# Optimization experiments

Measured on AMD Instinct MI355X. Metric: run time of the kernel, lower is better.

## Reference

```python
import jax, jax.numpy as jnp
import numpy as np
from jax import lax

EPS = 1e-3  # Keras BatchNormalization default epsilon
DN = ('NHWC', 'HWIO', 'NHWC')


def _bn(x, gamma, beta, mean, var):
    inv = gamma * lax.rsqrt(var + EPS)
    return x * inv + (beta - mean * inv)


def setup_inputs() -> dict:
    key = jax.random.key(0)
    ks = jax.random.split(key, 5)
    B, H, W, C = 32, 56, 56, 256
    G, CG = 32, 4  # cardinality, channels per group
    CM = G * CG    # 128 mid channels
    x = jax.random.normal(ks[0], (B, H, W, C), jnp.float32)
    # 32 branch 1x1 convs (256->4 each) stacked -> one 256->128 conv
    w1 = jax.random.normal(ks[1], (1, 1, C, CM), jnp.float32) * 0.05
    b1 = jnp.zeros((CM,), jnp.float32)
    g1 = jnp.ones((CM,), jnp.float32)
    be1 = jnp.zeros((CM,), jnp.float32)
    m1 = jnp.zeros((CM,), jnp.float32)
    v1 = jnp.ones((CM,), jnp.float32)
    # 32 branch 3x3 convs (4->4 each) stacked -> grouped conv kernel [3,3,4,128]
    w2 = jax.random.normal(ks[2], (3, 3, CG, CM), jnp.float32) * 0.1
    b2 = jnp.zeros((CM,), jnp.float32)
    g2 = jnp.ones((CM,), jnp.float32)
    be2 = jnp.zeros((CM,), jnp.float32)
    m2 = jnp.zeros((CM,), jnp.float32)
    v2 = jnp.ones((CM,), jnp.float32)
    # final 1x1 conv 128 -> 256
    w3 = jax.random.normal(ks[3], (1, 1, CM, C), jnp.float32) * 0.05
    b3 = jnp.zeros((C,), jnp.float32)
    return dict(x=x, w1=w1, b1=b1, g1=g1, be1=be1, m1=m1, v1=v1,
                w2=w2, b2=b2, g2=g2, be2=be2, m2=m2, v2=v2,
                w3=w3, b3=b3)


def reference(x, w1, b1, g1, be1, m1, v1, w2, b2, g2, be2, m2, v2, w3, b3):
    # branch 1x1 convs fused: conv 256 -> 128
    h = lax.conv_general_dilated(x, w1, (1, 1), 'SAME', dimension_numbers=DN) + b1
    h = jax.nn.relu(_bn(h, g1, be1, m1, v1))
    # branch 3x3 convs fused: grouped conv, 32 groups of 4 channels
    h = lax.conv_general_dilated(h, w2, (1, 1), 'SAME', dimension_numbers=DN,
                                 feature_group_count=32) + b2
    h = jax.nn.relu(_bn(h, g2, be2, m2, v2))
    # Dropout(0.2) is identity at inference
    # final 1x1 conv 128 -> 256, residual add, relu
    out = lax.conv_general_dilated(h, w3, (1, 1), 'SAME', dimension_numbers=DN) + b3
    return jax.nn.relu(out + x)
```

## Files before the change

### kernel.cpp

```cpp
#include <hip/hip_runtime.h>
#include <stdint.h>

typedef unsigned short u16;
typedef unsigned int   u32;
typedef __attribute__((ext_vector_type(8))) short bf16x8;
typedef __attribute__((ext_vector_type(4))) float f32x4;

#define EPS 1e-3f
#define NB 32
#define HW 56
#define CI 256
#define CM 128
#define PIX (NB*HW*HW)

__device__ __forceinline__ float asf(u32 i){ union{u32 u; float f;} t; t.u=i; return t.f; }
__device__ __forceinline__ u16 f2bf(float f){
  union{float f; u32 u;} t; t.f = f;
  u32 x = t.u;
  return (u16)((x + 0x7fffu + ((x>>16)&1u)) >> 16);
}

__global__ __launch_bounds__(256) void kprep(
    const float* __restrict__ w1, const float* __restrict__ b1, const float* __restrict__ g1,
    const float* __restrict__ be1, const float* __restrict__ m1, const float* __restrict__ v1,
    const float* __restrict__ b2, const float* __restrict__ g2,
    const float* __restrict__ be2, const float* __restrict__ m2, const float* __restrict__ v2,
    const float* __restrict__ w3,
    u16* __restrict__ w1t, u16* __restrict__ w3t,
    float* __restrict__ A1, float* __restrict__ B1,
    float* __restrict__ A2, float* __restrict__ B2){
  int i = blockIdx.x*256 + threadIdx.x;
  if (i < 32768){
    { int n = i >> 8, k = i & 255; w1t[i] = f2bf(w1[k*CM + n]); }
    { int n = i >> 7, k = i & 127; w3t[i] = f2bf(w3[k*CI + n]); }
  }
  if (i < 128){
    float s1 = g1[i] * rsqrtf(v1[i] + EPS);
    A1[i] = s1;
    B1[i] = b1[i]*s1 + be1[i] - m1[i]*s1;
    float s2 = g2[i] * rsqrtf(v2[i] + EPS);
    A2[i] = s2;
    B2[i] = b2[i]*s2 + be2[i] - m2[i]*s2;
  }
}

#define K1_LS 72
__global__ __launch_bounds__(256) void k1(const float* __restrict__ x,
    const u16* __restrict__ w1t, const float* __restrict__ A1v,
    const float* __restrict__ B1v, u16* __restrict__ h1){
  __shared__ __align__(16) char smem[64*K1_LS*2 + 128*K1_LS*2];
  u16* As = (u16*)smem;
  u16* Bs = (u16*)(smem + 64*K1_LS*2);
  const int tid  = threadIdx.x;
  const int lane = tid & 63, wv = tid >> 6;
  const int col  = lane & 15, quad = lane >> 4;
  const long p0 = (long)blockIdx.x * 64;
  f32x4 acc[4][2];
  #pragma unroll
  for (int a = 0; a < 4; a++){
    #pragma unroll
    for (int b = 0; b < 2; b++){ acc[a][b][0]=0.f; acc[a][b][1]=0.f; acc[a][b][2]=0.f; acc[a][b][3]=0.f; }
  }
  for (int kc = 0; kc < 4; kc++){
    #pragma unroll
    for (int r = 0; r < 4; r++){
      int idx = r*256 + tid;
      int m = idx >> 4, f4 = idx & 15;
      float4 v = *(const float4*)(x + (p0+m)*CI + kc*64 + f4*4);
      u32 lo = (u32)f2bf(v.x) | ((u32)f2bf(v.y) << 16);
      u32 hi = (u32)f2bf(v.z) | ((u32)f2bf(v.w) << 16);
      *(uint2*)(As + m*K1_LS + f4*4) = make_uint2(lo, hi);
    }
    #pragma unroll
    for (int r = 0; r < 4; r++){
      int idx = r*256 + tid;
      int n = idx >> 3, u4 = idx & 7;
      uint4 v = *(const uint4*)(w1t + n*CI + kc*64 + u4*8);
      *(uint4*)(Bs + n*K1_LS + u4*8) = v;
    }
    __syncthreads();
    #pragma unroll
    for (int ks = 0; ks < 2; ks++){
      bf16x8 af[4], bfr[2];
      #pragma unroll
      for (int mt = 0; mt < 4; mt++)
        af[mt] = *(const bf16x8*)(As + (mt*16 + col)*K1_LS + ks*32 + quad*8);
      #pragma unroll
      for (int nt = 0; nt < 2; nt++)
        bfr[nt] = *(const bf16x8*)(Bs + (wv*32 + nt*16 + col)*K1_LS + ks*32 + quad*8);
      #pragma unroll
      for (int mt = 0; mt < 4; mt++){
        #pragma unroll
        for (int nt = 0; nt < 2; nt++)
          acc[mt][nt] = __builtin_amdgcn_mfma_f32_16x16x32_bf16(af[mt], bfr[nt], acc[mt][nt], 0, 0, 0);
      }
    }
    __syncthreads();
  }
  u16* outw = (u16*)smem;
  #pragma unroll
  for (int nt = 0; nt < 2; nt++){
    int n = wv*32 + nt*16 + col;
    float a1 = A1v[n], b1v = B1v[n];
    #pragma unroll
    for (int mt = 0; mt < 4; mt++){
      #pragma unroll
      for (int reg = 0; reg < 4; reg++){
        int m = mt*16 + quad*4 + reg;
        outw[m*136 + n] = f2bf(fmaxf(acc[mt][nt][reg]*a1 + b1v, 0.f));
      }
    }
  }
  __syncthreads();
  #pragma unroll
  for (int r = 0; r < 4; r++){
    int idx = r*256 + tid;
    int m = idx >> 4, u4 = idx & 15;
    uint4 v = *(const uint4*)(outw + m*136 + u4*8);
    *(uint4*)(h1 + (p0+m)*CM + u4*8) = v;
  }
}

#define TW 58
#define CPAD 132
__global__ __launch_bounds__(256) void k2(const u16* __restrict__ h1,
    const float* __restrict__ wf2, const float* __restrict__ A2v,
    const float* __restrict__ B2v, u16* __restrict__ h2){
  __shared__ u16 tile[3][TW][CPAD];
  __shared__ float wsh[9*4*CM];
  const int tid = threadIdx.x;
  const int img = blockIdx.x / HW, y = blockIdx.x % HW;
  for (int i = tid; i < 4608; i += 256) wsh[i] = wf2[i];
  #pragma unroll
  for (int r = 0; r < 3; r++){
    const int yy = y + r - 1;
    if (yy < 0 || yy >= HW){
      u32* t = (u32*)&tile[r][0][0];
      for (int i = tid; i < TW*CPAD/2; i += 256) t[i] = 0u;
    } else {
      if (tid < CPAD){ tile[r][0][tid] = 0; tile[r][TW-1][tid] = 0; }
      const uint4* src = (const uint4*)(h1 + (size_t)(img*HW + yy)*HW*CM);
      for (int i = tid; i < 896; i += 256){
        uint4 v = src[i];
        int px = i >> 4, ch = (i & 15)*8;
        u16* d = &tile[r][px+1][ch];
        *(uint2*)d     = make_uint2(v.x, v.y);
        *(uint2*)(d+4) = make_uint2(v.z, v.w);
      }
    }
  }
  __syncthreads();
  const int lane = tid & 63, wv = tid >> 6;
  if (lane >= HW) return;
  const int px = lane;
  float acc[8][4];
  u16 ov[32];
  for (int gi = 0; gi < 8; gi++){
    const int cb = (wv*8 + gi)*4;
    float a0=0.f, a1=0.f, a2=0.f, a3=0.f;
    #pragma unroll
    for (int ky = 0; ky < 3; ky++){
      #pragma unroll
      for (int kx = 0; kx < 3; kx++){
        const u16* hp = &tile[ky][px+kx][cb];
        uint2 hv = *(const uint2*)hp;
        float i0 = asf(hv.x<<16), i1 = asf(hv.x&0xffff0000u);
        float i2 = asf(hv.y<<16), i3 = asf(hv.y&0xffff0000u);
        const float* wp = &wsh[(size_t)((ky*3+kx)*4)*CM + cb];
        float4 w0 = *(const float4*)(wp);
        float4 w1 = *(const float4*)(wp+CM);
        float4 w2 = *(const float4*)(wp+2*CM);
        float4 w3 = *(const float4*)(wp+3*CM);
        a0 += i0*w0.x + i1*w1.x + i2*w2.x + i3*w3.x;
        a1 += i0*w0.y + i1*w1.y + i2*w2.y + i3*w3.y;
        a2 += i0*w0.z + i1*w1.z + i2*w2.z + i3*w3.z;
        a3 += i0*w0.w + i1*w1.w + i2*w2.w + i3*w3.w;
      }
    }
    acc[gi][0]=a0; acc[gi][1]=a1; acc[gi][2]=a2; acc[gi][3]=a3;
  }
  const long p = (long)(img*HW + y)*HW + px;
  #pragma unroll
  for (int gi = 0; gi < 8; gi++){
    #pragma unroll
    for (int co = 0; co < 4; co++){
      int c = wv*32 + gi*4 + co;
      ov[gi*4+co] = f2bf(fmaxf(acc[gi][co]*A2v[c] + B2v[c], 0.f));
    }
  }
  u16* op = h2 + p*CM + wv*32;
  #pragma unroll
  for (int q = 0; q < 4; q++){
    uint4 pk;
    pk.x = (u32)ov[q*8+0] | ((u32)ov[q*8+1]<<16);
    pk.y = (u32)ov[q*8+2] | ((u32)ov[q*8+3]<<16);
    pk.z = (u32)ov[q*8+4] | ((u32)ov[q*8+5]<<16);
    pk.w = (u32)ov[q*8+6] | ((u32)ov[q*8+7]<<16);
    *(uint4*)(op + q*8) = pk;
  }
}

#define K3_LS 136
__global__ __launch_bounds__(256) void k3(const u16* __restrict__ h2,
    const u16* __restrict__ w3t, const float* __restrict__ b3,
    const float* __restrict__ x, float* __restrict__ out){
  __shared__ __align__(16) char smem[64*K3_LS*2 + 128*K3_LS*2];
  u16* As = (u16*)smem;
  u16* Bs = (u16*)(smem + 64*K3_LS*2);
  const int tid  = threadIdx.x;
  const int lane = tid & 63, wv = tid >> 6;
  const int col  = lane & 15, quad = lane >> 4;
  const long p0 = (long)blockIdx.x * 64;
  const int n0 = blockIdx.y * 128;
  #pragma unroll
  for (int r = 0; r < 4; r++){
    int idx = r*256 + tid;
    int m = idx >> 4, u4 = idx & 15;
    uint4 v = *(const uint4*)(h2 + (p0+m)*CM + u4*8);
    *(uint4*)(As + m*K3_LS + u4*8) = v;
  }
  #pragma unroll
  for (int r = 0; r < 8; r++){
    int idx = r*256 + tid;
    int n = idx >> 4, u4 = idx & 15;
    uint4 v = *(const uint4*)(w3t + (size_t)(n0+n)*CM + u4*8);
    *(uint4*)(Bs + n*K3_LS + u4*8) = v;
  }
  __syncthreads();
  f32x4 acc[4][2];
  #pragma unroll
  for (int a = 0; a < 4; a++){
    #pragma unroll
    for (int b = 0; b < 2; b++){ acc[a][b][0]=0.f; acc[a][b][1]=0.f; acc[a][b][2]=0.f; acc[a][b][3]=0.f; }
  }
  #pragma unroll
  for (int ks = 0; ks < 4; ks++){
    bf16x8 af[4], bfr[2];
    #pragma unroll
    for (int mt = 0; mt < 4; mt++)
      af[mt] = *(const bf16x8*)(As + (mt*16 + col)*K3_LS + ks*32 + quad*8);
    #pragma unroll
    for (int nt = 0; nt < 2; nt++)
      bfr[nt] = *(const bf16x8*)(Bs + (wv*32 + nt*16 + col)*K3_LS + ks*32 + quad*8);
    #pragma unroll
    for (int mt = 0; mt < 4; mt++){
      #pragma unroll
      for (int nt = 0; nt < 2; nt++)
        acc[mt][nt] = __builtin_amdgcn_mfma_f32_16x16x32_bf16(af[mt], bfr[nt], acc[mt][nt], 0, 0, 0);
    }
  }
  __syncthreads();
  float* outb = (float*)smem;
  #pragma unroll
  for (int nt = 0; nt < 2; nt++){
    int nl = wv*32 + nt*16 + col;
    float bb = b3[n0 + nl];
    #pragma unroll
    for (int mt = 0; mt < 4; mt++){
      #pragma unroll
      for (int reg = 0; reg < 4; reg++){
        int m = mt*16 + quad*4 + reg;
        outb[m*132 + nl] = acc[mt][nt][reg] + bb;
      }
    }
  }
  __syncthreads();
  #pragma unroll
  for (int r = 0; r < 8; r++){
    int idx = r*256 + tid;
    int m = idx >> 5, f4 = idx & 31;
    float4 pre = *(const float4*)(outb + m*132 + f4*4);
    const float* xr = x + (p0+m)*CI + n0 + f4*4;
    float4 xv = *(const float4*)xr;
    float4 o;
    o.x = fmaxf(pre.x + xv.x, 0.f);
    o.y = fmaxf(pre.y + xv.y, 0.f);
    o.z = fmaxf(pre.z + xv.z, 0.f);
    o.w = fmaxf(pre.w + xv.w, 0.f);
    *(float4*)(out + (p0+m)*CI + n0 + f4*4) = o;
  }
}

extern "C" void kernel_launch(void* const* d_in, const int* in_sizes, int n_in,
                              void* d_out, int out_size, void* d_ws, size_t ws_size,
                              hipStream_t stream){
  (void)in_sizes; (void)n_in; (void)out_size; (void)ws_size;
  const float* x   = (const float*)d_in[0];
  const float* w1  = (const float*)d_in[1];
  const float* b1  = (const float*)d_in[2];
  const float* g1  = (const float*)d_in[3];
  const float* be1 = (const float*)d_in[4];
  const float* m1  = (const float*)d_in[5];
  const float* v1  = (const float*)d_in[6];
  const float* w2  = (const float*)d_in[7];
  const float* b2  = (const float*)d_in[8];
  const float* g2  = (const float*)d_in[9];
  const float* be2 = (const float*)d_in[10];
  const float* m2  = (const float*)d_in[11];
  const float* v2  = (const float*)d_in[12];
  const float* w3  = (const float*)d_in[13];
  const float* b3  = (const float*)d_in[14];

  char* ws = (char*)d_ws;
  u16* h1 = (u16*)ws;
  u16* h2 = (u16*)(ws + (size_t)PIX*CM*2);
  u16* w1t = (u16*)(ws + (size_t)PIX*CM*4);
  u16* w3t = w1t + 32768;
  float* A1 = (float*)(w3t + 32768);
  float* B1 = A1 + 128;
  float* A2 = B1 + 128;
  float* B2 = A2 + 128;

  kprep<<<128, 256, 0, stream>>>(w1,b1,g1,be1,m1,v1,b2,g2,be2,m2,v2,w3,
                                 w1t,w3t,A1,B1,A2,B2);
  k1<<<PIX/64, 256, 0, stream>>>(x, w1t, A1, B1, h1);
  k2<<<NB*HW, 256, 0, stream>>>(h1, w2, A2, B2, h2);
  k3<<<dim3(PIX/64, 2), 256, 0, stream>>>(h2, w3t, b3, x, (float*)d_out);
}
```

Baseline: 292.5 us.

## Fuse grouped 3x3 conv with final 1x1 conv and enlarge k1 tile

Merges the grouped 3x3 conv and the final 1x1 conv into one kernel. Each 512-thread block computes two image rows of h2 into shared memory and feeds them straight into MFMA for the 128->256 conv plus the residual add. This removes the h2 round trip through global memory and one launch. k1 also moves from 64 to 128 pixels per block to reuse the weights more. The fused kernel needs about 108 KB of LDS and more registers, so occupancy is lower, and the w3 B-fragments are read directly from global memory.

```diff
diff --git a/kernel.cpp b/kernel.cpp
--- a/kernel.cpp
+++ b/kernel.cpp
@@ -48,22 +48,21 @@
 __global__ __launch_bounds__(256) void k1(const float* __restrict__ x,
     const u16* __restrict__ w1t, const float* __restrict__ A1v,
     const float* __restrict__ B1v, u16* __restrict__ h1){
-  __shared__ __align__(16) char smem[64*K1_LS*2 + 128*K1_LS*2];
+  __shared__ __align__(16) char smem[128*K1_LS*2 * 2];
   u16* As = (u16*)smem;
-  u16* Bs = (u16*)(smem + 64*K1_LS*2);
+  u16* Bs = (u16*)(smem + 128*K1_LS*2);
   const int tid  = threadIdx.x;
   const int lane = tid & 63, wv = tid >> 6;
   const int col  = lane & 15, quad = lane >> 4;
-  const long p0 = (long)blockIdx.x * 64;
-  f32x4 acc[4][2];
-  #pragma unroll
-  for (int a = 0; a < 4; a++){
+  const long p0 = (long)blockIdx.x * 128;
+  f32x4 acc[8][2];
+  #pragma unroll
+  for (int a = 0; a < 8; a++)
     #pragma unroll
     for (int b = 0; b < 2; b++){ acc[a][b][0]=0.f; acc[a][b][1]=0.f; acc[a][b][2]=0.f; acc[a][b][3]=0.f; }
-  }
   for (int kc = 0; kc < 4; kc++){
     #pragma unroll
-    for (int r = 0; r < 4; r++){
+    for (int r = 0; r < 8; r++){
       int idx = r*256 + tid;
       int m = idx >> 4, f4 = idx & 15;
       float4 v = *(const float4*)(x + (p0+m)*CI + kc*64 + f4*4);
@@ -81,19 +80,18 @@
     __syncthreads();
     #pragma unroll
     for (int ks = 0; ks < 2; ks++){
-      bf16x8 af[4], bfr[2];
-      #pragma unroll
-      for (int mt = 0; mt < 4; mt++)
-        af[mt] = *(const bf16x8*)(As + (mt*16 + col)*K1_LS + ks*32 + quad*8);
+      bf16x8 af[8], bfr[2];
       #pragma unroll
       for (int nt = 0; nt < 2; nt++)
         bfr[nt] = *(const bf16x8*)(Bs + (wv*32 + nt*16 + col)*K1_LS + ks*32 + quad*8);
       #pragma unroll
-      for (int mt = 0; mt < 4; mt++){
+      for (int mt = 0; mt < 8; mt++)
+        af[mt] = *(const bf16x8*)(As + (mt*16 + col)*K1_LS + ks*32 + quad*8);
+      #pragma unroll
+      for (int mt = 0; mt < 8; mt++)
         #pragma unroll
         for (int nt = 0; nt < 2; nt++)
           acc[mt][nt] = __builtin_amdgcn_mfma_f32_16x16x32_bf16(af[mt], bfr[nt], acc[mt][nt], 0, 0, 0);
-      }
     }
     __syncthreads();
   }
@@ -103,17 +101,16 @@
     int n = wv*32 + nt*16 + col;
     float a1 = A1v[n], b1v = B1v[n];
     #pragma unroll
-    for (int mt = 0; mt < 4; mt++){
+    for (int mt = 0; mt < 8; mt++)
       #pragma unroll
       for (int reg = 0; reg < 4; reg++){
         int m = mt*16 + quad*4 + reg;
         outw[m*136 + n] = f2bf(fmaxf(acc[mt][nt][reg]*a1 + b1v, 0.f));
       }
-    }
   }
   __syncthreads();
   #pragma unroll
-  for (int r = 0; r < 4; r++){
+  for (int r = 0; r < 8; r++){
     int idx = r*256 + tid;
     int m = idx >> 4, u4 = idx & 15;
     uint4 v = *(const uint4*)(outw + m*136 + u4*8);
@@ -121,163 +118,156 @@
   }
 }
 
-#define TW 58
-#define CPAD 132
-__global__ __launch_bounds__(256) void k2(const u16* __restrict__ h1,
-    const float* __restrict__ wf2, const float* __restrict__ A2v,
-    const float* __restrict__ B2v, u16* __restrict__ h2){
-  __shared__ u16 tile[3][TW][CPAD];
-  __shared__ float wsh[9*4*CM];
+#define LSH1 132
+#define LSH2 136
+__global__ __launch_bounds__(512) void k23(const u16* __restrict__ h1,
+    const float* __restrict__ w2, const float* __restrict__ A2v,
+    const float* __restrict__ B2v, const u16* __restrict__ w3t,
+    const float* __restrict__ b3, const float* __restrict__ x,
+    float* __restrict__ out){
+  __shared__ __align__(16) char smem[59136 + 112*LSH2*2 + 4608*4];
+  u16*  tile = (u16*)smem;
+  u16*  h2t  = (u16*)(smem + 59136);
+  float* wsh = (float*)(smem + 59136 + 112*LSH2*2);
+  float* pre = (float*)smem;
+
   const int tid = threadIdx.x;
-  const int img = blockIdx.x / HW, y = blockIdx.x % HW;
-  for (int i = tid; i < 4608; i += 256) wsh[i] = wf2[i];
-  #pragma unroll
-  for (int r = 0; r < 3; r++){
-    const int yy = y + r - 1;
-    if (yy < 0 || yy >= HW){
-      u32* t = (u32*)&tile[r][0][0];
-      for (int i = tid; i < TW*CPAD/2; i += 256) t[i] = 0u;
-    } else {
-      if (tid < CPAD){ tile[r][0][tid] = 0; tile[r][TW-1][tid] = 0; }
-      const uint4* src = (const uint4*)(h1 + (size_t)(img*HW + yy)*HW*CM);
-      for (int i = tid; i < 896; i += 256){
-        uint4 v = src[i];
-        int px = i >> 4, ch = (i & 15)*8;
-        u16* d = &tile[r][px+1][ch];
-        *(uint2*)d     = make_uint2(v.x, v.y);
-        *(uint2*)(d+4) = make_uint2(v.z, v.w);
+  const int g0 = blockIdx.x * 2;
+  const int y0 = g0 % HW;
+  const long p0 = (long)g0 * HW;
+
+  for (int i = tid; i < 1152; i += 512)
+    ((float4*)wsh)[i] = ((const float4*)w2)[i];
+  #pragma unroll
+  for (int r = 0; r < 4; r++){
+    const int yy = y0 + r - 1;
+    const bool valid = (yy >= 0 && yy < HW);
+    const uint4* src = (const uint4*)(h1 + (long)(g0 - y0 + yy)*HW*CM);
+    for (int i = tid; i < 896; i += 512){
+      uint4 v = make_uint4(0u,0u,0u,0u);
+      if (valid) v = src[i];
+      int px = i >> 4, ch = (i & 15)*8;
+      u16* d = tile + (r*HW + px)*LSH1 + ch;
+      *(uint2*)d     = make_uint2(v.x, v.y);
+      *(uint2*)(d+4) = make_uint2(v.z, v.w);
+    }
+  }
+  __syncthreads();
+
+  {
+    const int q   = tid >> 7;
+    const int pos = tid & 127;
+    if (pos < 112){
+      const int r_out = (pos >= HW) ? 1 : 0;
+      const int px = pos - r_out*HW;
+      int ixo[3]; u32 mk[3];
+      #pragma unroll
+      for (int kx = 0; kx < 3; kx++){
+        int c = px + kx - 1;
+        ixo[kx] = (c < 0 ? 0 : (c > 55 ? 55 : c)) * LSH1;
+        mk[kx] = (c >= 0 && c < HW) ? 0xffffffffu : 0u;
       }
+      float acc[8][4];
+      #pragma unroll
+      for (int gi = 0; gi < 8; gi++){
+        const int cb = (q*8 + gi)*4;
+        float a0=0.f, a1=0.f, a2=0.f, a3=0.f;
+        #pragma unroll
+        for (int ky = 0; ky < 3; ky++){
+          const u16* trow = tile + (r_out+ky)*HW*LSH1 + cb;
+          #pragma unroll
+          for (int kx = 0; kx < 3; kx++){
+            uint2 hv = *(const uint2*)(trow + ixo[kx]);
+            u32 hx = hv.x & mk[kx], hy = hv.y & mk[kx];
+            float i0 = asf(hx<<16), i1 = asf(hx&0xffff0000u);
+            float i2 = asf(hy<<16), i3 = asf(hy&0xffff0000u);
+            const float* wp = wsh + ((ky*3+kx)*4)*CM + cb;
+            float4 w0 = *(const float4*)(wp);
+            float4 w1 = *(const float4*)(wp+CM);
+            float4 wq2 = *(const float4*)(wp+2*CM);
+            float4 wq3 = *(const float4*)(wp+3*CM);
+            a0 += i0*w0.x + i1*w1.x + i2*wq2.x + i3*wq3.x;
+            a1 += i0*w0.y + i1*w1.y + i2*wq2.y + i3*wq3.y;
+            a2 += i0*w0.z + i1*w1.z + i2*wq2.z + i3*wq3.z;
+            a3 += i0*w0.w + i1*w1.w + i2*wq2.w + i3*wq3.w;
+          }
+        }
+        acc[gi][0]=a0; acc[gi][1]=a1; acc[gi][2]=a2; acc[gi][3]=a3;
+      }
+      u16 ov[32];
+      #pragma unroll
+      for (int gi = 0; gi < 8; gi++)
+        #pragma unroll
+        for (int co = 0; co < 4; co++){
+          int c = q*32 + gi*4 + co;
+          ov[gi*4+co] = f2bf(fmaxf(acc[gi][co]*A2v[c] + B2v[c], 0.f));
+        }
+      u16* op = h2t + pos*LSH2 + q*32;
+      #pragma unroll
+      for (int v4 = 0; v4 < 4; v4++){
+        uint4 pk;
+        pk.x = (u32)ov[v4*8+0] | ((u32)ov[v4*8+1]<<16);
+        pk.y = (u32)ov[v4*8+2] | ((u32)ov[v4*8+3]<<16);
+        pk.z = (u32)ov[v4*8+4] | ((u32)ov[v4*8+5]<<16);
+        pk.w = (u32)ov[v4*8+6] | ((u32)ov[v4*8+7]<<16);
+        *(uint4*)(op + v4*8) = pk;
+      }
     }
   }
   __syncthreads();
-  const int lane = tid & 63, wv = tid >> 6;
-  if (lane >= HW) return;
-  const int px = lane;
-  float acc[8][4];
-  u16 ov[32];
-  for (int gi = 0; gi < 8; gi++){
-    const int cb = (wv*8 + gi)*4;
-    float a0=0.f, a1=0.f, a2=0.f, a3=0.f;
-    #pragma unroll
-    for (int ky = 0; ky < 3; ky++){
-      #pragma unroll
-      for (int kx = 0; kx < 3; kx++){
-        const u16* hp = &tile[ky][px+kx][cb];
-        uint2 hv = *(const uint2*)hp;
-        float i0 = asf(hv.x<<16), i1 = asf(hv.x&0xffff0000u);
-        float i2 = asf(hv.y<<16), i3 = asf(hv.y&0xffff0000u);
-        const float* wp = &wsh[(size_t)((ky*3+kx)*4)*CM + cb];
-        float4 w0 = *(const float4*)(wp);
-        float4 w1 = *(const float4*)(wp+CM);
-        float4 w2 = *(const float4*)(wp+2*CM);
-        float4 w3 = *(const float4*)(wp+3*CM);
-        a0 += i0*w0.x + i1*w1.x + i2*w2.x + i3*w3.x;
-        a1 += i0*w0.y + i1*w1.y + i2*w2.y + i3*w3.y;
-        a2 += i0*w0.z + i1*w1.z + i2*w2.z + i3*w3.z;
-        a3 += i0*w0.w + i1*w1.w + i2*w2.w + i3*w3.w;
-      }
-    }
-    acc[gi][0]=a0; acc[gi][1]=a1; acc[gi][2]=a2; acc[gi][3]=a3;
-  }
-  const long p = (long)(img*HW + y)*HW + px;
-  #pragma unroll
-  for (int gi = 0; gi < 8; gi++){
-    #pragma unroll
-    for (int co = 0; co < 4; co++){
-      int c = wv*32 + gi*4 + co;
-      ov[gi*4+co] = f2bf(fmaxf(acc[gi][co]*A2v[c] + B2v[c], 0.f));
-    }
-  }
-  u16* op = h2 + p*CM + wv*32;
-  #pragma unroll
-  for (int q = 0; q < 4; q++){
-    uint4 pk;
-    pk.x = (u32)ov[q*8+0] | ((u32)ov[q*8+1]<<16);
-    pk.y = (u32)ov[q*8+2] | ((u32)ov[q*8+3]<<16);
-    pk.z = (u32)ov[q*8+4] | ((u32)ov[q*8+5]<<16);
-    pk.w = (u32)ov[q*8+6] | ((u32)ov[q*8+7]<<16);
-    *(uint4*)(op + q*8) = pk;
-  }
-}
-
-#define K3_LS 136
-__global__ __launch_bounds__(256) void k3(const u16* __restrict__ h2,
-    const u16* __restrict__ w3t, const float* __restrict__ b3,
-    const float* __restrict__ x, float* __restrict__ out){
-  __shared__ __align__(16) char smem[64*K3_LS*2 + 128*K3_LS*2];
-  u16* As = (u16*)smem;
-  u16* Bs = (u16*)(smem + 64*K3_LS*2);
-  const int tid  = threadIdx.x;
+
   const int lane = tid & 63, wv = tid >> 6;
   const int col  = lane & 15, quad = lane >> 4;
-  const long p0 = (long)blockIdx.x * 64;
-  const int n0 = blockIdx.y * 128;
-  #pragma unroll
-  for (int r = 0; r < 4; r++){
-    int idx = r*256 + tid;
-    int m = idx >> 4, u4 = idx & 15;
-    uint4 v = *(const uint4*)(h2 + (p0+m)*CM + u4*8);
-    *(uint4*)(As + m*K3_LS + u4*8) = v;
-  }
-  #pragma unroll
-  for (int r = 0; r < 8; r++){
-    int idx = r*256 + tid;
-    int n = idx >> 4, u4 = idx & 15;
-    uint4 v = *(const uint4*)(w3t + (size_t)(n0+n)*CM + u4*8);
-    *(uint4*)(Bs + n*K3_LS + u4*8) = v;
-  }
-  __syncthreads();
-  f32x4 acc[4][2];
-  #pragma unroll
-  for (int a = 0; a < 4; a++){
-    #pragma unroll
-    for (int b = 0; b < 2; b++){ acc[a][b][0]=0.f; acc[a][b][1]=0.f; acc[a][b][2]=0.f; acc[a][b][3]=0.f; }
-  }
-  #pragma unroll
-  for (int ks = 0; ks < 4; ks++){
-    bf16x8 af[4], bfr[2];
-    #pragma unroll
-    for (int mt = 0; mt < 4; mt++)
-      af[mt] = *(const bf16x8*)(As + (mt*16 + col)*K3_LS + ks*32 + quad*8);
+  const int nb = (wv & 3) * 32;
+  const int nh = wv >> 2;
+  const int ng = nh*128 + nb;
+  f32x4 acc3[7][2];
+  #pragma unroll
+  for (int a = 0; a < 7; a++)
+    #pragma unroll
+    for (int b = 0; b < 2; b++){ acc3[a][b][0]=0.f; acc3[a][b][1]=0.f; acc3[a][b][2]=0.f; acc3[a][b][3]=0.f; }
+  float bias[2] = { b3[ng + col], b3[ng + 16 + col] };
+  #pragma unroll
+  for (int kc = 0; kc < 4; kc++){
+    bf16x8 bfr[2];
     #pragma unroll
     for (int nt = 0; nt < 2; nt++)
-      bfr[nt] = *(const bf16x8*)(Bs + (wv*32 + nt*16 + col)*K3_LS + ks*32 + quad*8);
-    #pragma unroll
-    for (int mt = 0; mt < 4; mt++){
+      bfr[nt] = *(const bf16x8*)(w3t + (size_t)(ng + nt*16 + col)*CM + kc*32 + quad*8);
+    #pragma unroll
+    for (int mt = 0; mt < 7; mt++){
+      bf16x8 af = *(const bf16x8*)(h2t + (mt*16 + col)*LSH2 + kc*32 + quad*8);
       #pragma unroll
       for (int nt = 0; nt < 2; nt++)
-        acc[mt][nt] = __builtin_amdgcn_mfma_f32_16x16x32_bf16(af[mt], bfr[nt], acc[mt][nt], 0, 0, 0);
-    }
-  }
-  __syncthreads();
-  float* outb = (float*)smem;
-  #pragma unroll
-  for (int nt = 0; nt < 2; nt++){
-    int nl = wv*32 + nt*16 + col;
-    float bb = b3[n0 + nl];
-    #pragma unroll
-    for (int mt = 0; mt < 4; mt++){
-      #pragma unroll
-      for (int reg = 0; reg < 4; reg++){
-        int m = mt*16 + quad*4 + reg;
-        outb[m*132 + nl] = acc[mt][nt][reg] + bb;
-      }
-    }
-  }
-  __syncthreads();
-  #pragma unroll
-  for (int r = 0; r < 8; r++){
-    int idx = r*256 + tid;
-    int m = idx >> 5, f4 = idx & 31;
-    float4 pre = *(const float4*)(outb + m*132 + f4*4);
-    const float* xr = x + (p0+m)*CI + n0 + f4*4;
-    float4 xv = *(const float4*)xr;
-    float4 o;
-    o.x = fmaxf(pre.x + xv.x, 0.f);
-    o.y = fmaxf(pre.y + xv.y, 0.f);
-    o.z = fmaxf(pre.z + xv.z, 0.f);
-    o.w = fmaxf(pre.w + xv.w, 0.f);
-    *(float4*)(out + (p0+m)*CI + n0 + f4*4) = o;
+        acc3[mt][nt] = __builtin_amdgcn_mfma_f32_16x16x32_bf16(af, bfr[nt], acc3[mt][nt], 0, 0, 0);
+    }
+  }
+  #pragma unroll
+  for (int h = 0; h < 2; h++){
+    if (nh == h){
+      #pragma unroll
+      for (int mt = 0; mt < 7; mt++)
+        #pragma unroll
+        for (int nt = 0; nt < 2; nt++)
+          #pragma unroll
+          for (int reg = 0; reg < 4; reg++){
+            int m = mt*16 + quad*4 + reg;
+            pre[m*132 + nb + nt*16 + col] = acc3[mt][nt][reg] + bias[nt];
+          }
+    }
+    __syncthreads();
+    for (int i = tid; i < 3584; i += 512){
+      int m = i >> 5, f4 = i & 31;
+      float4 pv = *(const float4*)(pre + m*132 + f4*4);
+      const float* xr = x + (p0+m)*CI + h*128 + f4*4;
+      float4 xv = *(const float4*)xr;
+      float4 o;
+      o.x = fmaxf(pv.x + xv.x, 0.f);
+      o.y = fmaxf(pv.y + xv.y, 0.f);
+      o.z = fmaxf(pv.z + xv.z, 0.f);
+      o.w = fmaxf(pv.w + xv.w, 0.f);
+      *(float4*)(out + (p0+m)*CI + h*128 + f4*4) = o;
+    }
+    __syncthreads();
   }
 }
 
@@ -302,9 +292,8 @@
   const float* b3  = (const float*)d_in[14];
 
   char* ws = (char*)d_ws;
-  u16* h1 = (u16*)ws;
-  u16* h2 = (u16*)(ws + (size_t)PIX*CM*2);
-  u16* w1t = (u16*)(ws + (size_t)PIX*CM*4);
+  u16* h1  = (u16*)ws;
+  u16* w1t = (u16*)(ws + (size_t)PIX*CM*2);
   u16* w3t = w1t + 32768;
   float* A1 = (float*)(w3t + 32768);
   float* B1 = A1 + 128;
@@ -313,7 +302,6 @@
 
   kprep<<<128, 256, 0, stream>>>(w1,b1,g1,be1,m1,v1,b2,g2,be2,m2,v2,w3,
                                  w1t,w3t,A1,B1,A2,B2);
-  k1<<<PIX/64, 256, 0, stream>>>(x, w1t, A1, B1, h1);
-  k2<<<NB*HW, 256, 0, stream>>>(h1, w2, A2, B2, h2);
-  k3<<<dim3(PIX/64, 2), 256, 0, stream>>>(h2, w3t, b3, x, (float*)d_out);
-}
+  k1<<<PIX/128, 256, 0, stream>>>(x, w1t, A1, B1, h1);
+  k23<<<NB*HW/2, 512, 0, stream>>>(h1, w2, A2, B2, w3t, b3, x, (float*)d_out);
+}
```

After: 294.5 us. No clear change (+0.7%).
